# Performance work log

Measured on AMD Instinct MI355X. Metric: run time of the kernel, lower is better.

Reference implementation:

```python
import jax, jax.numpy as jnp
import numpy as np

INTER, COMMAND, MOTOR = 128, 64, 32
UNITS = MOTOR + COMMAND + INTER  # neuron order: motor, command, inter
SENSORY = 64
SENSORY_FANOUT, INTER_FANOUT = 16, 16
REC_CMD_SYN, MOTOR_FANIN = 128, 16
OUTPUT_LEN = 32
ODE_UNFOLDS = 6
EPS = 1e-8


def _build_wiring(rng):
    adj = np.zeros((UNITS, UNITS), np.float32)      # [pre, post]
    sadj = np.zeros((SENSORY, UNITS), np.float32)   # [sensory, post]
    motor = np.arange(0, MOTOR)
    command = np.arange(MOTOR, MOTOR + COMMAND)
    inter = np.arange(MOTOR + COMMAND, UNITS)
    pol = lambda: rng.choice(np.asarray([-1.0, 1.0], np.float32))
    for s in range(SENSORY):
        for d in rng.choice(inter, size=SENSORY_FANOUT, replace=False):
            sadj[s, d] = pol()
    for i in inter:
        for d in rng.choice(command, size=INTER_FANOUT, replace=False):
            adj[i, d] = pol()
    for _ in range(REC_CMD_SYN):
        adj[rng.choice(command), rng.choice(command)] = pol()
    for m in motor:
        for s in rng.choice(command, size=MOTOR_FANIN, replace=False):
            adj[s, m] = pol()
    return adj, sadj


def setup_inputs() -> dict:
    rng = np.random.default_rng(0)
    adj, sadj = _build_wiring(rng)
    u = lambda lo, hi, shp: jnp.asarray(rng.uniform(lo, hi, shp), jnp.float32)
    inp = {
        'inputs': jnp.asarray(rng.standard_normal((32, 32, SENSORY)), jnp.float32),
        'input_w': jnp.ones((SENSORY,), jnp.float32),
        'input_b': jnp.zeros((SENSORY,), jnp.float32),
        'sensory_mu': u(0.3, 0.8, (SENSORY, UNITS)),
        'sensory_sigma': u(3.0, 8.0, (SENSORY, UNITS)),
        'sensory_w': u(0.001, 1.0, (SENSORY, UNITS)),
        'sensory_erev': jnp.asarray(sadj),
        'sensory_mask': jnp.asarray(np.abs(sadj)),
        'mu': u(0.3, 0.8, (UNITS, UNITS)),
        'sigma': u(3.0, 8.0, (UNITS, UNITS)),
        'w': u(0.001, 1.0, (UNITS, UNITS)),
        'erev': jnp.asarray(adj),
        'mask': jnp.asarray(np.abs(adj)),
        'gleak': u(0.001, 1.0, (UNITS,)),
        'vleak': u(-0.2, 0.2, (UNITS,)),
        'cm': u(0.4, 0.6, (UNITS,)),
        'output_w': jnp.ones((MOTOR,), jnp.float32),
        'output_b': jnp.zeros((MOTOR,), jnp.float32),
        'dense_w': jnp.asarray(rng.standard_normal((MOTOR, OUTPUT_LEN)) / np.sqrt(MOTOR), jnp.float32),
        'dense_b': jnp.zeros((OUTPUT_LEN,), jnp.float32),
    }
    return inp


def reference(inputs, input_w, input_b, sensory_mu, sensory_sigma, sensory_w,
              sensory_erev, sensory_mask, mu, sigma, w, erev, mask,
              gleak, vleak, cm, output_w, output_b, dense_w, dense_b):
    # affine input mapping (per sensory feature)
    x = inputs * input_w + input_b  # [B,T,S]
    cm_t = cm * ODE_UNFOLDS        # cm / (elapsed_time / unfolds), elapsed_time=1

    def step(v, xt):  # v: [B,U], xt: [B,S]
        s_act = sensory_w * jax.nn.sigmoid(sensory_sigma * (xt[:, :, None] - sensory_mu)) * sensory_mask  # [B,S,U]
        w_num_s = jnp.sum(s_act * sensory_erev, axis=1)  # [B,U]
        w_den_s = jnp.sum(s_act, axis=1)
        for _ in range(ODE_UNFOLDS):
            w_act = w * jax.nn.sigmoid(sigma * (v[:, :, None] - mu)) * mask  # [B,U,U]
            num = cm_t * v + gleak * vleak + jnp.sum(w_act * erev, axis=1) + w_num_s
            den = cm_t + gleak + jnp.sum(w_act, axis=1) + w_den_s
            v = num / (den + EPS)
        return v, v

    v0 = jnp.zeros((x.shape[0], UNITS), x.dtype)
    _, vs = jax.lax.scan(step, v0, jnp.moveaxis(x, 1, 0))  # [T,B,U]
    motor = vs[..., :MOTOR] * output_w + output_b          # [T,B,M]
    out = jnp.einsum('tbm,mo->bto', motor, dense_w) + dense_b  # [B,T,OUT]
    return out
```

## Files before the change

### kernel.cpp

```cpp
#include <hip/hip_runtime.h>


#define U_N 224
#define S_N 64
#define T_N 32
#define M_N 32
#define C_N 64
#define I_N 128
#define O_N 32
#define NUF 6
#define TJT (T_N * NUF)
#define ELLS 24
#define ELLC 64
#define CCK 12
#define PFD 16
#define EPSV 1e-8f
#define L2E  1.44269504088896340736f

#define OFF_S2I   0
#define OFF_I2C   12288
#define OFF_CC    28672
#define OFF_M2T   31744
#define OFF_CNT   33792
#define OFF_CONST 34112
#define OFF_DYN   34816

#if __has_builtin(__builtin_amdgcn_rcpf)
#define RCPF(x) __builtin_amdgcn_rcpf(x)
#else
#define RCPF(x) (1.0f / (x))
#endif
#if __has_builtin(__builtin_amdgcn_exp2f)
#define EXP2F(x) __builtin_amdgcn_exp2f(x)
#else
#define EXP2F(x) exp2f(x)
#endif

__device__ __forceinline__ float bfu(unsigned short b) {
    return __uint_as_float(((unsigned int)b) << 16);
}
template <bool BF>
__device__ __forceinline__ float ld(const void* p, int i) {
    if (BF) return bfu(((const unsigned short*)p)[i]);
    return ((const float*)p)[i];
}
__device__ __forceinline__ unsigned short f2bf(float f) {
    unsigned int u = __float_as_uint(f);
    u += 0x7FFFu + ((u >> 16) & 1u);
    return (unsigned short)(u >> 16);
}
template <bool BF>
__device__ __forceinline__ void st_out(void* p, int i, float v) {
    if (BF) ((unsigned short*)p)[i] = f2bf(v);
    else    ((float*)p)[i] = v;
}
__device__ __forceinline__ float sigm2(float t) {
    return RCPF(1.0f + EXP2F(t));
}

template <bool BF>
__device__ void build_body(float* ws,
    const void* g_smu, const void* g_ssig, const void* g_sw,
    const void* g_serev, const void* g_smask,
    const void* g_mu, const void* g_sig, const void* g_w,
    const void* g_erev, const void* g_mask,
    const void* g_gleak, const void* g_vleak, const void* g_cm)
{
    const int tid = threadIdx.x;
    const int gt = blockIdx.x * 256 + tid;
    const int stride = gridDim.x * 256;
    int* cnt = (int*)(ws + OFF_CNT);
    if (gt < U_N) {
        float g = ld<BF>(g_gleak, gt);
        float cmt = ld<BF>(g_cm, gt) * (float)NUF;
        ws[OFF_CONST + gt] = cmt;
        ws[OFF_CONST + U_N + gt] = g * ld<BF>(g_vleak, gt);
        ws[OFF_CONST + 2 * U_N + gt] = cmt + g + EPSV;
    }
    float4* ws4 = (float4*)ws;
    for (int idx = gt; idx < U_N * U_N; idx += stride) {
        if (ld<BF>(g_mask, idx) != 0.f) {
            int pre = idx / U_N, post = idx - pre * U_N;
            float sg = ld<BF>(g_sig, idx) * L2E;
            float smu = sg * ld<BF>(g_mu, idx);
            float we = ld<BF>(g_w, idx) * ld<BF>(g_erev, idx);
            if (post < M_N) {
                int s = atomicAdd(&cnt[256 + post], 1);
                if (s < 16) ws4[OFF_M2T / 4 + s * M_N + post] =
                    make_float4(sg, smu, we, __int_as_float(pre - M_N));
            } else if (post < M_N + C_N) {
                int c = post - M_N;
                if (pre >= M_N + C_N) {
                    int s = atomicAdd(&cnt[128 + c], 1);
                    if (s < ELLC) ws4[OFF_I2C / 4 + c * ELLC + s] =
                        make_float4(sg, smu, we, __int_as_float(pre - M_N - C_N));
                } else {
                    int s = atomicAdd(&cnt[192 + c], 1);
                    if (s < CCK) ws4[OFF_CC / 4 + c * CCK + s] =
                        make_float4(sg, smu, we, __int_as_float(pre - M_N));
                }
            }
        }
    }
    for (int idx = gt; idx < S_N * U_N; idx += stride) {
        if (ld<BF>(g_smask, idx) != 0.f) {
            int pre = idx / U_N;
            int i = (idx - pre * U_N) - (M_N + C_N);
            if (i >= 0) {
                int s = atomicAdd(&cnt[i], 1);
                if (s < ELLS) {
                    float sg = ld<BF>(g_ssig, idx) * L2E;
                    ws4[OFF_S2I / 4 + i * ELLS + s] = make_float4(
                        sg, sg * ld<BF>(g_smu, idx),
                        ld<BF>(g_sw, idx) * ld<BF>(g_serev, idx),
                        __int_as_float(pre));
                }
            }
        }
    }
}

__global__ __launch_bounds__(256) void k_build(
    const void* sniff, const void* g_smu, const void* g_ssig, const void* g_sw,
    const void* g_serev, const void* g_smask, const void* g_mu,
    const void* g_sig, const void* g_w, const void* g_erev, const void* g_mask,
    const void* g_gleak, const void* g_vleak, const void* g_cm, float* ws)
{
    unsigned w0 = *(const unsigned int*)sniff;
    if (w0 == 0x3F800000u)
        build_body<false>(ws, g_smu, g_ssig, g_sw, g_serev, g_smask, g_mu,
                          g_sig, g_w, g_erev, g_mask, g_gleak, g_vleak, g_cm);
    else
        build_body<true>(ws, g_smu, g_ssig, g_sw, g_serev, g_smask, g_mu,
                         g_sig, g_w, g_erev, g_mask, g_gleak, g_vleak, g_cm);
}

template <bool BF>
__device__ void inter_body(float* ws, const void* g_inputs,
                           const void* g_in_w, const void* g_in_b)
{
    __shared__ float xs[T_N][S_N];
    const int tid = threadIdx.x, b = blockIdx.x;
    for (int g = tid; g < T_N * S_N; g += 256) {
        int t = g >> 6, s = g & 63;
        xs[t][s] = ld<BF>(g_inputs, (b * T_N + t) * S_N + s) *
                       ld<BF>(g_in_w, s) + ld<BF>(g_in_b, s);
    }
    const int iOwn = tid >> 1, lane2 = tid & 1;
    const float4* ws4 = (const float4*)ws;
    int n = ((const int*)(ws + OFF_CNT))[iOwn];
    float pSg[12], pMu[12], pW[12]; int pPre[12];
    #pragma unroll
    for (int k = 0; k < 12; ++k) {
        int s = lane2 + (k << 1);
        if (s < n) {
            float4 q = ws4[OFF_S2I / 4 + iOwn * ELLS + s];
            pSg[k] = q.x; pMu[k] = q.y; pW[k] = q.z; pPre[k] = __float_as_int(q.w);
        } else { pSg[k] = 0.f; pMu[k] = 0.f; pW[k] = 0.f; pPre[k] = 0; }
    }
    int kB = (n + 1) >> 1;
    #pragma unroll
    for (int off = 1; off < 64; off <<= 1) {
        int o = __shfl_xor(kB, off, 64); kB = (o > kB) ? o : kB;
    }
    kB = __builtin_amdgcn_readfirstlane(kB);
    const float cmtI = ws[OFF_CONST + M_N + C_N + iOwn];
    const float baseI = ws[OFF_CONST + U_N + M_N + C_N + iOwn];
    const float cgeI = ws[OFF_CONST + 2 * U_N + M_N + C_N + iOwn];
    __syncthreads();
    float* wVI = ws + OFF_DYN + (size_t)b * TJT * I_N;
    float vi = 0.f;
    for (int t = 0; t < T_N; ++t) {
        float accS = 0.f, accD = 0.f;
        #pragma unroll
        for (int k = 0; k < 12; ++k) {
            if (k < kB) {
                float xv = xs[t][pPre[k]];
                float sg = sigm2(fmaf(-pSg[k], xv, pMu[k]));
                float wv = pW[k] * sg;
                accS += wv; accD += fabsf(wv);
            }
        }
        accS += __shfl_xor(accS, 1, 2);
        accD += __shfl_xor(accD, 1, 2);
        float rden = RCPF(cgeI + accD);
        float A = cmtI * rden, Bv = (baseI + accS) * rden;
        #pragma unroll
        for (int j = 0; j < NUF; ++j) {
            if (lane2 == 0) wVI[(t * NUF + j) * I_N + iOwn] = vi;
            vi = fmaf(A, vi, Bv);
        }
    }
}

__global__ __launch_bounds__(256) void k_inter(
    const void* sniff, const void* g_inputs, const void* g_in_w,
    const void* g_in_b, float* ws)
{
    unsigned w0 = *(const unsigned int*)sniff;
    if (w0 == 0x3F800000u) inter_body<false>(ws, g_inputs, g_in_w, g_in_b);
    else                   inter_body<true>(ws, g_inputs, g_in_w, g_in_b);
}

__global__ __launch_bounds__(512) void k_i2c(float* ws)
{
    __shared__ float  vi_s[8 * I_N];
    __shared__ float2 scs[8 * C_N];
    const int tid = threadIdx.x, b = blockIdx.x, tj0 = blockIdx.y * 8;
    const int B = gridDim.x;
    const float* wVI = ws + OFF_DYN + ((size_t)b * TJT + tj0) * I_N;
    float2* wSC = (float2*)(ws + OFF_DYN + (size_t)B * TJT * I_N) +
                  ((size_t)b * (TJT + PFD) + tj0) * C_N;
    for (int g = tid; g < 8 * I_N; g += 512) vi_s[g] = wVI[g];
    const int cOwn = tid >> 3, lane8 = tid & 7;
    int n = ((const int*)(ws + OFF_CNT))[128 + cOwn];
    const float4* ws4 = (const float4*)ws;
    float pSg[8], pMu[8], pW[8]; int pPre[8];
    #pragma unroll
    for (int k = 0; k < 8; ++k) {
        int s = lane8 + (k << 3);
        if (s < n) {
            float4 q = ws4[OFF_I2C / 4 + cOwn * ELLC + s];
            pSg[k] = q.x; pMu[k] = q.y; pW[k] = q.z; pPre[k] = __float_as_int(q.w);
        } else { pSg[k] = 0.f; pMu[k] = 0.f; pW[k] = 0.f; pPre[k] = 0; }
    }
    int kB = (n + 7) >> 3;
    #pragma unroll
    for (int off = 1; off < 64; off <<= 1) {
        int o = __shfl_xor(kB, off, 64); kB = (o > kB) ? o : kB;
    }
    kB = __builtin_amdgcn_readfirstlane(kB);
    __syncthreads();
    for (int r = 0; r < 8; ++r) {
        const float* row = vi_s + r * I_N;
        float accS = 0.f, accD = 0.f;
        #pragma unroll
        for (int k = 0; k < 8; ++k) {
            if (k < kB) {
                float vv = row[pPre[k]];
                float sg = sigm2(fmaf(-pSg[k], vv, pMu[k]));
                float wv = pW[k] * sg;
                accS += wv; accD += fabsf(wv);
            }
        }
        accS += __shfl_xor(accS, 1, 8);
        accS += __shfl_xor(accS, 2, 8);
        accS += __shfl_xor(accS, 4, 8);
        accD += __shfl_xor(accD, 1, 8);
        accD += __shfl_xor(accD, 2, 8);
        accD += __shfl_xor(accD, 4, 8);
        if (lane8 == 0) scs[r * C_N + cOwn] = make_float2(accS, accD);
    }
    __syncthreads();
    wSC[tid] = scs[tid];
}

template <bool BF>
__device__ void cmdmo_body(float* ws, const void* g_ow, const void* g_ob,
                           const void* g_dw, const void* g_db,
                           void* __restrict__ g_out)
{
    __shared__ float  ct[TJT][C_N];
    __shared__ float2 mabc[24][M_N];
    __shared__ float  moutS[T_N][M_N];
    __shared__ float  dwS[M_N * O_N];
    const int tid = threadIdx.x, b = blockIdx.x, B = gridDim.x;
    for (int g = tid; g < M_N * O_N; g += 256) dwS[g] = ld<BF>(g_dw, g);

    if (tid < C_N) {
        const int lane = tid;
        int n = ((const int*)(ws + OFF_CNT))[192 + lane];
        const float4* ws4 = (const float4*)ws;
        float pSg[CCK], pMu[CCK], pW[CCK]; int pPre[CCK];
        #pragma unroll
        for (int k = 0; k < CCK; ++k) {
            if (k < n) {
                float4 q = ws4[OFF_CC / 4 + lane * CCK + k];
                pSg[k] = q.x; pMu[k] = q.y; pW[k] = q.z;
                pPre[k] = __float_as_int(q.w);
            } else { pSg[k] = 0.f; pMu[k] = 0.f; pW[k] = 0.f; pPre[k] = 0; }
        }
        int ccK = n;
        #pragma unroll
        for (int off = 1; off < 64; off <<= 1) {
            int o = __shfl_xor(ccK, off, 64); ccK = (o > ccK) ? o : ccK;
        }
        ccK = __builtin_amdgcn_readfirstlane(ccK);
        const float cmtC = ws[OFF_CONST + M_N + lane];
        const float baseC = ws[OFF_CONST + U_N + M_N + lane];
        const float cgeC = ws[OFF_CONST + 2 * U_N + M_N + lane];
        const float2* wSC = (const float2*)(ws + OFF_DYN + (size_t)B * TJT * I_N) +
                            (size_t)b * (TJT + PFD) * C_N + lane;
        float2 pf[PFD];
        #pragma unroll
        for (int k = 0; k < PFD; ++k) pf[k] = wSC[(size_t)k * C_N];
        float vC = 0.f;
        for (int tj0 = 0; tj0 < TJT; tj0 += PFD) {
            #pragma unroll
            for (int k = 0; k < PFD; ++k) {
                float2 sd = pf[k];
                pf[k] = wSC[(size_t)(tj0 + PFD + k) * C_N];
                ct[tj0 + k][lane] = vC;
                float accS = 0.f, accD = 0.f;
                #pragma unroll
                for (int kk = 0; kk < CCK; ++kk) {
                    if (kk < ccK) {
                        float vv = __shfl(vC, pPre[kk], 64);
                        float sg = sigm2(fmaf(-pSg[kk], vv, pMu[kk]));
                        float wv = pW[kk] * sg;
                        accS += wv; accD += fabsf(wv);
                    }
                }
                vC = fmaf(cmtC, vC, baseC + sd.x + accS) *
                     RCPF(cgeC + sd.y + accD);
            }
        }
    }
    __syncthreads();

    const int m = tid & 31, grp = tid >> 5;
    const float4* ws4 = (const float4*)ws;
    float4 q[16];
    #pragma unroll
    for (int k = 0; k < 16; ++k) q[k] = ws4[OFF_M2T / 4 + k * M_N + m];
    const float cmtM = ws[OFF_CONST + m];
    const float baseM = ws[OFF_CONST + U_N + m];
    const float cgeM = ws[OFF_CONST + 2 * U_N + m];
    float owR = 0.f, obR = 0.f, vM = 0.f;
    if (tid < M_N) { owR = ld<BF>(g_ow, tid); obR = ld<BF>(g_ob, tid); }
    for (int r = 0; r < 8; ++r) {
        #pragma unroll
        for (int z = 0; z < 3; ++z) {
            int tl = grp * 3 + z;
            const float* crow = ct[r * 24 + tl];
            float accS = 0.f, accD = 0.f;
            #pragma unroll
            for (int k = 0; k < 16; ++k) {
                float vv = crow[__float_as_int(q[k].w)];
                float sg = sigm2(fmaf(-q[k].x, vv, q[k].y));
                float wv = q[k].z * sg;
                accS += wv; accD += fabsf(wv);
            }
            float rden = RCPF(cgeM + accD);
            mabc[tl][m] = make_float2(cmtM * rden, (baseM + accS) * rden);
        }
        __syncthreads();
        if (tid < M_N) {
            #pragma unroll
            for (int tt = 0; tt < 4; ++tt) {
                #pragma unroll
                for (int j = 0; j < NUF; ++j) {
                    float2 ab = mabc[tt * NUF + j][tid];
                    vM = fmaf(ab.x, vM, ab.y);
                }
                moutS[r * 4 + tt][tid] = fmaf(vM, owR, obR);
            }
        }
        __syncthreads();
    }

    for (int g = tid; g < T_N * O_N; g += 256) {
        int t = g >> 5, o = g & 31;
        float acc = ld<BF>(g_db, o);
        #pragma unroll 8
        for (int mm = 0; mm < M_N; ++mm)
            acc += moutS[t][mm] * dwS[mm * O_N + o];
        st_out<BF>(g_out, (b * T_N + t) * O_N + o, acc);
    }
}

__global__ __launch_bounds__(256) void k_cmdmo(
    const void* sniff, float* ws, const void* g_ow, const void* g_ob,
    const void* g_dw, const void* g_db, void* __restrict__ g_out)
{
    unsigned w0 = *(const unsigned int*)sniff;
    if (w0 == 0x3F800000u) cmdmo_body<false>(ws, g_ow, g_ob, g_dw, g_db, g_out);
    else                   cmdmo_body<true>(ws, g_ow, g_ob, g_dw, g_db, g_out);
}

#define MONO_NT 640
#define CH  4
#define NCH (T_N / CH)
#define TJ  (CH * NUF)
#define KI  8
#define KS  6

struct SmemM {
    float cmt[U_N], base[U_N], cge[U_N];
    float4 m2t[16][M_N];
    float mout[T_N][M_N];
    union {
        struct {
            unsigned short ell_c[C_N][ELLC];
            unsigned short ell_s[I_N][ELLS];
            float4 cc[C_N][CCK];
            int cnt_c[C_N], cnt_s[I_N], cnt_cc[C_N], cnt_m[M_N];
        } b;
        struct {
            float  x[CH][S_N];
            float  Vi[TJ][I_N];
            float2 sc[2][TJ][C_N];
            float  ctraj[TJ][C_N];
            float2 mAB[TJ][M_N];
        } r;
    } u;
};

template <bool BF>
__device__ void mono_body(SmemM& sm,
    const void* g_inputs, const void* g_in_w, const void* g_in_b,
    const void* g_smu, const void* g_ssig, const void* g_sw,
    const void* g_serev, const void* g_smask,
    const void* g_mu, const void* g_sig, const void* g_w,
    const void* g_erev, const void* g_mask,
    const void* g_gleak, const void* g_vleak, const void* g_cm,
    const void* g_ow, const void* g_ob, const void* g_dw, const void* g_db,
    void* __restrict__ g_out)
{
    const int tid = threadIdx.x;
    const int b = blockIdx.x;
    const int p = tid - 64;
    const bool wp = (p >= 0 && p < 512);
    const bool isMo = (p >= 512 && p < 512 + M_N);

    if (tid < U_N) {
        float g = ld<BF>(g_gleak, tid);
        float cmt = ld<BF>(g_cm, tid) * (float)NUF;
        sm.cmt[tid] = cmt;
        sm.base[tid] = g * ld<BF>(g_vleak, tid);
        sm.cge[tid] = cmt + g + EPSV;
    }
    if (tid < C_N) { sm.u.b.cnt_c[tid] = 0; sm.u.b.cnt_cc[tid] = 0; }
    if (tid < I_N) sm.u.b.cnt_s[tid] = 0;
    if (tid < M_N) sm.u.b.cnt_m[tid] = 0;
    if (tid < 512) sm.m2t[tid >> 5][tid & 31] =
        make_float4(0.f, 0.f, 0.f, __int_as_float(0));
    __syncthreads();

    for (int idx = tid; idx < U_N * U_N; idx += MONO_NT) {
        if (ld<BF>(g_mask, idx) != 0.f) {
            int pre = idx / U_N;
            int post = idx - pre * U_N;
            if (post < M_N) {
                int s = atomicAdd(&sm.u.b.cnt_m[post], 1);
                if (s < 16) {
                    float sg = ld<BF>(g_sig, idx) * L2E;
                    float we = ld<BF>(g_w, idx) * ld<BF>(g_erev, idx);
                    sm.m2t[s][post] = make_float4(sg, sg * ld<BF>(g_mu, idx),
                                                  we, __int_as_float(pre - M_N));
                }
            } else if (post < M_N + C_N) {
                int c = post - M_N;
                if (pre >= M_N + C_N) {
                    int s = atomicAdd(&sm.u.b.cnt_c[c], 1);
                    if (s < ELLC) sm.u.b.ell_c[c][s] = (unsigned short)idx;
                } else {
                    int s = atomicAdd(&sm.u.b.cnt_cc[c], 1);
                    if (s < CCK) {
                        float sg = ld<BF>(g_sig, idx) * L2E;
                        float we = ld<BF>(g_w, idx) * ld<BF>(g_erev, idx);
                        sm.u.b.cc[c][s] = make_float4(sg, sg * ld<BF>(g_mu, idx),
                                                      we, __int_as_float(pre - M_N));
                    }
                }
            }
        }
    }
    for (int idx = tid; idx < S_N * U_N; idx += MONO_NT) {
        if (ld<BF>(g_smask, idx) != 0.f) {
            int pre = idx / U_N;
            int i = (idx - pre * U_N) - (M_N + C_N);
            if (i >= 0) {
                int s = atomicAdd(&sm.u.b.cnt_s[i], 1);
                if (s < ELLS) sm.u.b.ell_s[i][s] = (unsigned short)idx;
            }
        }
    }
    __syncthreads();

    const int cOwn = wp ? (p >> 3) : 0, lane8 = wp ? (p & 7) : 0;
    const int iOwn = wp ? (p >> 2) : 0, lane4 = wp ? (p & 3) : 0;
    float iSg[KI], iMu[KI], iW[KI]; int iPre[KI]; int kWi = 0;
    {
        int n = wp ? min(sm.u.b.cnt_c[cOwn], ELLC) : 0;
        #pragma unroll
        for (int k = 0; k < KI; ++k) {
            int s = lane8 + (k << 3);
            iSg[k] = 0.f; iMu[k] = 0.f; iW[k] = 0.f; iPre[k] = 0;
            if (s < n) {
                int flat = sm.u.b.ell_c[cOwn][s];
                float sg = ld<BF>(g_sig, flat) * L2E;
                iSg[k] = sg; iMu[k] = sg * ld<BF>(g_mu, flat);
                iW[k] = ld<BF>(g_w, flat) * ld<BF>(g_erev, flat);
                iPre[k] = flat / U_N - (M_N + C_N);
            }
        }
        kWi = (n + 7) >> 3;
    }
    float sSg[KS], sMu[KS], sW[KS]; int sPre[KS]; int kWs = 0;
    {
        int n = wp ? min(sm.u.b.cnt_s[iOwn], ELLS) : 0;
        #pragma unroll
        for (int k = 0; k < KS; ++k) {
            int s = lane4 + (k << 2);
            sSg[k] = 0.f; sMu[k] = 0.f; sW[k] = 0.f; sPre[k] = 0;
            if (s < n) {
                int flat = sm.u.b.ell_s[iOwn][s];
                float sg = ld<BF>(g_ssig, flat) * L2E;
                sSg[k] = sg; sMu[k] = sg * ld<BF>(g_smu, flat);
                sW[k] = ld<BF>(g_sw, flat) * ld<BF>(g_serev, flat);
                sPre[k] = flat / U_N;
            }
        }
        kWs = (n + 3) >> 2;
    }
    #pragma unroll
    for (int off = 1; off < 64; off <<= 1) {
        int o = __shfl_xor(kWi, off, 64); kWi = (o > kWi) ? o : kWi;
        int q2 = __shfl_xor(kWs, off, 64); kWs = (q2 > kWs) ? q2 : kWs;
    }
    kWi = __builtin_amdgcn_readfirstlane(kWi);
    kWs = __builtin_amdgcn_readfirstlane(kWs);

    float kSg[CCK], kMu[CCK], kW[CCK]; int kPre[CCK]; int ccK = 0;
    float cmtC = 0.f, baseC = 0.f, cgeC = 0.f;
    if (tid < C_N) {
        int n = min(sm.u.b.cnt_cc[tid], CCK);
        #pragma unroll
        for (int k = 0; k < CCK; ++k) {
            if (k < n) {
                float4 q3 = sm.u.b.cc[tid][k];
                kSg[k] = q3.x; kMu[k] = q3.y; kW[k] = q3.z;
                kPre[k] = __float_as_int(q3.w);
            } else { kSg[k] = 0.f; kMu[k] = 0.f; kW[k] = 0.f; kPre[k] = 0; }
        }
        ccK = n;
        #pragma unroll
        for (int off = 1; off < 64; off <<= 1) {
            int o = __shfl_xor(ccK, off, 64);
            ccK = (o > ccK) ? o : ccK;
        }
        ccK = __builtin_amdgcn_readfirstlane(ccK);
        cmtC = sm.cmt[M_N + tid]; baseC = sm.base[M_N + tid];
        cgeC = sm.cge[M_N + tid];
    }
    const float cmtI = sm.cmt[M_N + C_N + iOwn];
    const float baseI = sm.base[M_N + C_N + iOwn];
    const float cgeI = sm.cge[M_N + C_N + iOwn];
    float owR = 0.f, obR = 0.f;
    if (isMo) { owR = ld<BF>(g_ow, p - 512); obR = ld<BF>(g_ob, p - 512); }
    __syncthreads();

    if (wp && p < CH * S_N) {
        int tt = p >> 6, s = p & 63;
        sm.u.r.x[tt][s] = ld<BF>(g_inputs, (b * T_N + tt) * S_N + s) *
                              ld<BF>(g_in_w, s) + ld<BF>(g_in_b, s);
    }
    __syncthreads();

    float vInt = 0.f;
    float vCmd = 0.f;
    float vMot = 0.f;

    for (int i = 0; i <= NCH; ++i) {
        if (tid < C_N) {
            if (i >= 1) {
                const float2* scb = &sm.u.r.sc[(i - 1) & 1][0][0];
                for (int tj = 0; tj < TJ / 2; ++tj) {
                    sm.u.r.ctraj[tj][tid] = vCmd;
                    float accS = 0.f, accD = 0.f;
                    #pragma unroll
                    for (int k = 0; k < CCK; ++k) {
                        if (k < ccK) {
                            float vv = __shfl(vCmd, kPre[k], 64);
                            float sg = sigm2(fmaf(-kSg[k], vv, kMu[k]));
                            float wv = kW[k] * sg;
                            accS += wv; accD += fabsf(wv);
                        }
                    }
                    float2 sd = scb[tj * C_N + tid];
                    vCmd = fmaf(cmtC, vCmd, baseC + sd.x + accS) *
                           RCPF(cgeC + sd.y + accD);
                }
            }
        } else if (wp) {
            if (i < NCH) {
                float vi = vInt;
                for (int tt = 0; tt < CH; ++tt) {
                    float accS = 0.f, accD = 0.f;
                    #pragma unroll
                    for (int k = 0; k < KS; ++k) {
                        if (k < kWs) {
                            float xv = sm.u.r.x[tt][sPre[k]];
                            float sg = sigm2(fmaf(-sSg[k], xv, sMu[k]));
                            float wv = sW[k] * sg;
                            accS += wv; accD += fabsf(wv);
                        }
                    }
                    accS += __shfl_xor(accS, 1, 4); accS += __shfl_xor(accS, 2, 4);
                    accD += __shfl_xor(accD, 1, 4); accD += __shfl_xor(accD, 2, 4);
                    float rden = RCPF(cgeI + accD);
                    float A = cmtI * rden;
                    float Bv = (baseI + accS) * rden;
                    #pragma unroll
                    for (int j = 0; j < NUF; ++j) {
                        if (lane4 == 0) sm.u.r.Vi[tt * NUF + j][iOwn] = vi;
                        vi = fmaf(A, vi, Bv);
                    }
                }
                vInt = vi;
            }
        } else if (isMo && i >= 2) {
            int m = p - 512, c = i - 2;
            for (int tt = 0; tt < CH; ++tt) {
                #pragma unroll
                for (int j = 0; j < NUF; ++j) {
                    float2 ab = sm.u.r.mAB[tt * NUF + j][m];
                    vMot = fmaf(ab.x, vMot, ab.y);
                }
                sm.mout[c * CH + tt][m] = fmaf(vMot, owR, obR);
            }
        }
        __syncthreads();

        if (tid < C_N) {
            if (i >= 1) {
                const float2* scb = &sm.u.r.sc[(i - 1) & 1][0][0];
                for (int tj = TJ / 2; tj < TJ; ++tj) {
                    sm.u.r.ctraj[tj][tid] = vCmd;
                    float accS = 0.f, accD = 0.f;
                    #pragma unroll
                    for (int k = 0; k < CCK; ++k) {
                        if (k < ccK) {
                            float vv = __shfl(vCmd, kPre[k], 64);
                            float sg = sigm2(fmaf(-kSg[k], vv, kMu[k]));
                            float wv = kW[k] * sg;
                            accS += wv; accD += fabsf(wv);
                        }
                    }
                    float2 sd = scb[tj * C_N + tid];
                    vCmd = fmaf(cmtC, vCmd, baseC + sd.x + accS) *
                           RCPF(cgeC + sd.y + accD);
                }
            }
        } else if (wp) {
            if (i < NCH) {
                float2* scw = &sm.u.r.sc[i & 1][0][0];
                for (int tj = 0; tj < TJ; ++tj) {
                    const float* vrow = &sm.u.r.Vi[tj][0];
                    float accS = 0.f, accD = 0.f;
                    #pragma unroll
                    for (int k = 0; k < KI; ++k) {
                        if (k < kWi) {
                            float vv = vrow[iPre[k]];
                            float sg = sigm2(fmaf(-iSg[k], vv, iMu[k]));
                            float wv = iW[k] * sg;
                            accS += wv; accD += fabsf(wv);
                        }
                    }
                    accS += __shfl_xor(accS, 1, 8);
                    accS += __shfl_xor(accS, 2, 8);
                    accS += __shfl_xor(accS, 4, 8);
                    accD += __shfl_xor(accD, 1, 8);
                    accD += __shfl_xor(accD, 2, 8);
                    accD += __shfl_xor(accD, 4, 8);
                    if (lane8 == 0) scw[tj * C_N + cOwn] = make_float2(accS, accD);
                }
            }
            if (i + 1 < NCH && p < CH * S_N) {
                int tt = p >> 6, s = p & 63;
                sm.u.r.x[tt][s] =
                    ld<BF>(g_inputs, (b * T_N + (i + 1) * CH + tt) * S_N + s) *
                        ld<BF>(g_in_w, s) + ld<BF>(g_in_b, s);
            }
        }
        __syncthreads();

        if (i >= 1) {
            for (int g = tid; g < TJ * M_N; g += MONO_NT) {
                int tj = g >> 5, m = g & 31;
                const float* crow = &sm.u.r.ctraj[tj][0];
                float accS = 0.f, accD = 0.f;
                #pragma unroll
                for (int k = 0; k < 16; ++k) {
                    float4 q4 = sm.m2t[k][m];
                    float vv = crow[__float_as_int(q4.w)];
                    float sg = sigm2(fmaf(-q4.x, vv, q4.y));
                    float wv = q4.z * sg;
                    accS += wv; accD += fabsf(wv);
                }
                float rden = RCPF(sm.cge[m] + accD);
                sm.u.r.mAB[tj][m] = make_float2(sm.cmt[m] * rden,
                                                (sm.base[m] + accS) * rden);
            }
        }
        __syncthreads();
    }

    if (isMo) {
        int m = p - 512, c = NCH - 1;
        for (int tt = 0; tt < CH; ++tt) {
            #pragma unroll
            for (int j = 0; j < NUF; ++j) {
                float2 ab = sm.u.r.mAB[tt * NUF + j][m];
                vMot = fmaf(ab.x, vMot, ab.y);
            }
            sm.mout[c * CH + tt][m] = fmaf(vMot, owR, obR);
        }
    }
    __syncthreads();

    for (int g = tid; g < T_N * O_N; g += MONO_NT) {
        int t = g >> 5, o = g & 31;
        float acc = ld<BF>(g_db, o);
        #pragma unroll 8
        for (int m = 0; m < M_N; ++m)
            acc += sm.mout[t][m] * ld<BF>(g_dw, m * O_N + o);
        st_out<BF>(g_out, (b * T_N + t) * O_N + o, acc);
    }
}

__global__ __launch_bounds__(MONO_NT) void ncp_mono(
    const void* i0,  const void* i1,  const void* i2,  const void* i3,
    const void* i4,  const void* i5,  const void* i6,  const void* i7,
    const void* i8,  const void* i9,  const void* i10, const void* i11,
    const void* i12, const void* i13, const void* i14, const void* i15,
    const void* i16, const void* i17, const void* i18, const void* i19,
    void* __restrict__ g_out)
{
    __shared__ SmemM sm;
    unsigned w0 = *(const unsigned int*)i1;
    if (w0 == 0x3F800000u)
        mono_body<false>(sm, i0, i1, i2, i3, i4, i5, i6, i7, i8, i9, i10, i11,
                         i12, i13, i14, i15, i16, i17, i18, i19, g_out);
    else
        mono_body<true>(sm, i0, i1, i2, i3, i4, i5, i6, i7, i8, i9, i10, i11,
                        i12, i13, i14, i15, i16, i17, i18, i19, g_out);
}

extern "C" void kernel_launch(void* const* d_in, const int* in_sizes, int n_in,
                              void* d_out, int out_size, void* d_ws, size_t ws_size,
                              hipStream_t stream) {
    (void)n_in; (void)out_size;
    const int B = in_sizes[0] / (T_N * S_N);
    float* ws = (float*)d_ws;
    const size_t req = ((size_t)OFF_DYN + (size_t)B * TJT * I_N +
                        (size_t)B * (TJT + PFD) * C_N * 2) * sizeof(float);
    if (d_ws != nullptr && ws_size >= req) {
        hipMemsetAsync((char*)d_ws + (size_t)OFF_CNT * sizeof(float), 0,
                       288 * sizeof(int), stream);
        k_build<<<dim3(16), dim3(256), 0, stream>>>(
            d_in[1], d_in[3], d_in[4], d_in[5], d_in[6], d_in[7], d_in[8],
            d_in[9], d_in[10], d_in[11], d_in[12], d_in[13], d_in[14],
            d_in[15], ws);
        k_inter<<<dim3(B), dim3(256), 0, stream>>>(
            d_in[1], d_in[0], d_in[1], d_in[2], ws);
        k_i2c<<<dim3(B, TJT / 8), dim3(512), 0, stream>>>(ws);
        k_cmdmo<<<dim3(B), dim3(256), 0, stream>>>(
            d_in[1], ws, d_in[16], d_in[17], d_in[18], d_in[19], d_out);
    } else {
        ncp_mono<<<dim3(B), dim3(MONO_NT), 0, stream>>>(
            d_in[0],  d_in[1],  d_in[2],  d_in[3],  d_in[4],  d_in[5],
            d_in[6],  d_in[7],  d_in[8],  d_in[9],  d_in[10], d_in[11],
            d_in[12], d_in[13], d_in[14], d_in[15], d_in[16], d_in[17],
            d_in[18], d_in[19], d_out);
    }
}
```

Measured before the change: 222.8 us.

## Stage command inputs in double-buffered LDS and restructure motor phase

The sequential command-neuron recurrence no longer uses a register prefetch ring from global memory. The other waves copy 48-step segments of precomputed sensory/inter contributions into double-buffered shared memory while wave 0 iterates. Neighbour voltages are now read from the shared ct array instead of cross-lane shuffles. The motor phase is rewritten to compute all per-step A/B coefficients in one parallel pass and then run the motor recurrence once, which removes eight rounds of block barriers. The build grid size also doubles. The trade-offs are LDS reads on the critical serial path in place of shuffles, and a larger shared-memory footprint.

```diff
diff --git a/kernel.cpp b/kernel.cpp
--- a/kernel.cpp
+++ b/kernel.cpp
@@ -10,10 +10,10 @@
 #define O_N 32
 #define NUF 6
 #define TJT (T_N * NUF)
+#define SEG 48
 #define ELLS 24
 #define ELLC 64
 #define CCK 12
-#define PFD 16
 #define EPSV 1e-8f
 #define L2E  1.44269504088896340736f
 
@@ -136,10 +136,10 @@
 }
 
 template <bool BF>
-__device__ void inter_body(float* ws, const void* g_inputs,
-                           const void* g_in_w, const void* g_in_b)
-{
-    __shared__ float xs[T_N][S_N];
+__device__ void inter_body(float (&xs)[T_N][S_N], float* ws,
+                           const void* g_inputs, const void* g_in_w,
+                           const void* g_in_b)
+{
     const int tid = threadIdx.x, b = blockIdx.x;
     for (int g = tid; g < T_N * S_N; g += 256) {
         int t = g >> 6, s = g & 63;
@@ -197,9 +197,10 @@
     const void* sniff, const void* g_inputs, const void* g_in_w,
     const void* g_in_b, float* ws)
 {
+    __shared__ float xs[T_N][S_N];
     unsigned w0 = *(const unsigned int*)sniff;
-    if (w0 == 0x3F800000u) inter_body<false>(ws, g_inputs, g_in_w, g_in_b);
-    else                   inter_body<true>(ws, g_inputs, g_in_w, g_in_b);
+    if (w0 == 0x3F800000u) inter_body<false>(xs, ws, g_inputs, g_in_w, g_in_b);
+    else                   inter_body<true>(xs, ws, g_inputs, g_in_w, g_in_b);
 }
 
 __global__ __launch_bounds__(512) void k_i2c(float* ws)
@@ -210,7 +211,7 @@
     const int B = gridDim.x;
     const float* wVI = ws + OFF_DYN + ((size_t)b * TJT + tj0) * I_N;
     float2* wSC = (float2*)(ws + OFF_DYN + (size_t)B * TJT * I_N) +
-                  ((size_t)b * (TJT + PFD) + tj0) * C_N;
+                  ((size_t)b * TJT + tj0) * C_N;
     for (int g = tid; g < 8 * I_N; g += 512) vi_s[g] = wVI[g];
     const int cOwn = tid >> 3, lane8 = tid & 7;
     int n = ((const int*)(ws + OFF_CNT))[128 + cOwn];
@@ -255,57 +256,67 @@
     wSC[tid] = scs[tid];
 }
 
+struct SmemC {
+    float ct[TJT][C_N];
+    union {
+        float2 sb[2][SEG][C_N];
+        float2 mAB[TJT][M_N];
+    } u;
+    float moutS[T_N][M_N];
+    float dwS[M_N * O_N];
+};
+
 template <bool BF>
-__device__ void cmdmo_body(float* ws, const void* g_ow, const void* g_ob,
-                           const void* g_dw, const void* g_db,
-                           void* __restrict__ g_out)
-{
-    __shared__ float  ct[TJT][C_N];
-    __shared__ float2 mabc[24][M_N];
-    __shared__ float  moutS[T_N][M_N];
-    __shared__ float  dwS[M_N * O_N];
+__device__ void cmdmo_body(SmemC& s, float* ws, const void* g_ow,
+                           const void* g_ob, const void* g_dw,
+                           const void* g_db, void* __restrict__ g_out)
+{
     const int tid = threadIdx.x, b = blockIdx.x, B = gridDim.x;
-    for (int g = tid; g < M_N * O_N; g += 256) dwS[g] = ld<BF>(g_dw, g);
-
+    const float2* wSC = (const float2*)(ws + OFF_DYN + (size_t)B * TJT * I_N) +
+                        (size_t)b * TJT * C_N;
+    for (int g = tid; g < M_N * O_N; g += 256) s.dwS[g] = ld<BF>(g_dw, g);
+    for (int g = tid; g < SEG * C_N; g += 256)
+        (&s.u.sb[0][0][0])[g] = wSC[g];
+
+    float pSg[CCK], pMu[CCK], pW[CCK]; int pPre[CCK]; int ccK = 0;
+    float cmtC = 0.f, baseC = 0.f, cgeC = 0.f;
     if (tid < C_N) {
-        const int lane = tid;
-        int n = ((const int*)(ws + OFF_CNT))[192 + lane];
+        int n = ((const int*)(ws + OFF_CNT))[192 + tid];
         const float4* ws4 = (const float4*)ws;
-        float pSg[CCK], pMu[CCK], pW[CCK]; int pPre[CCK];
         #pragma unroll
         for (int k = 0; k < CCK; ++k) {
             if (k < n) {
-                float4 q = ws4[OFF_CC / 4 + lane * CCK + k];
+                float4 q = ws4[OFF_CC / 4 + tid * CCK + k];
                 pSg[k] = q.x; pMu[k] = q.y; pW[k] = q.z;
                 pPre[k] = __float_as_int(q.w);
             } else { pSg[k] = 0.f; pMu[k] = 0.f; pW[k] = 0.f; pPre[k] = 0; }
         }
-        int ccK = n;
+        ccK = n;
         #pragma unroll
         for (int off = 1; off < 64; off <<= 1) {
             int o = __shfl_xor(ccK, off, 64); ccK = (o > ccK) ? o : ccK;
         }
         ccK = __builtin_amdgcn_readfirstlane(ccK);
-        const float cmtC = ws[OFF_CONST + M_N + lane];
-        const float baseC = ws[OFF_CONST + U_N + M_N + lane];
-        const float cgeC = ws[OFF_CONST + 2 * U_N + M_N + lane];
-        const float2* wSC = (const float2*)(ws + OFF_DYN + (size_t)B * TJT * I_N) +
-                            (size_t)b * (TJT + PFD) * C_N + lane;
-        float2 pf[PFD];
-        #pragma unroll
-        for (int k = 0; k < PFD; ++k) pf[k] = wSC[(size_t)k * C_N];
-        float vC = 0.f;
-        for (int tj0 = 0; tj0 < TJT; tj0 += PFD) {
-            #pragma unroll
-            for (int k = 0; k < PFD; ++k) {
-                float2 sd = pf[k];
-                pf[k] = wSC[(size_t)(tj0 + PFD + k) * C_N];
-                ct[tj0 + k][lane] = vC;
+        cmtC = ws[OFF_CONST + M_N + tid];
+        baseC = ws[OFF_CONST + U_N + M_N + tid];
+        cgeC = ws[OFF_CONST + 2 * U_N + M_N + tid];
+    }
+    __syncthreads();
+
+    float vC = 0.f;
+    for (int seg = 0; seg < 4; ++seg) {
+        if (tid < C_N) {
+            const int lane = tid;
+            const float2* scb = &s.u.sb[seg & 1][0][0];
+            for (int r = 0; r < SEG; ++r) {
+                const int tj = seg * SEG + r;
+                s.ct[tj][lane] = vC;
+                float2 sd = scb[r * C_N + lane];
                 float accS = 0.f, accD = 0.f;
                 #pragma unroll
                 for (int kk = 0; kk < CCK; ++kk) {
                     if (kk < ccK) {
-                        float vv = __shfl(vC, pPre[kk], 64);
+                        float vv = s.ct[tj][pPre[kk]];
                         float sg = sigm2(fmaf(-pSg[kk], vv, pMu[kk]));
                         float wv = pW[kk] * sg;
                         accS += wv; accD += fabsf(wv);
@@ -314,11 +325,15 @@
                 vC = fmaf(cmtC, vC, baseC + sd.x + accS) *
                      RCPF(cgeC + sd.y + accD);
             }
-        }
-    }
-    __syncthreads();
-
-    const int m = tid & 31, grp = tid >> 5;
+        } else if (seg < 3) {
+            float2* dst = &s.u.sb[(seg + 1) & 1][0][0];
+            const float2* src = wSC + (size_t)(seg + 1) * SEG * C_N;
+            for (int g = tid - 64; g < SEG * C_N; g += 192) dst[g] = src[g];
+        }
+        __syncthreads();
+    }
+
+    const int m = tid & 31;
     const float4* ws4 = (const float4*)ws;
     float4 q[16];
     #pragma unroll
@@ -326,45 +341,42 @@
     const float cmtM = ws[OFF_CONST + m];
     const float baseM = ws[OFF_CONST + U_N + m];
     const float cgeM = ws[OFF_CONST + 2 * U_N + m];
-    float owR = 0.f, obR = 0.f, vM = 0.f;
-    if (tid < M_N) { owR = ld<BF>(g_ow, tid); obR = ld<BF>(g_ob, tid); }
-    for (int r = 0; r < 8; ++r) {
-        #pragma unroll
-        for (int z = 0; z < 3; ++z) {
-            int tl = grp * 3 + z;
-            const float* crow = ct[r * 24 + tl];
-            float accS = 0.f, accD = 0.f;
+    for (int g = tid; g < TJT * M_N; g += 256) {
+        int tj = g >> 5;
+        const float* crow = s.ct[tj];
+        float accS = 0.f, accD = 0.f;
+        #pragma unroll
+        for (int k = 0; k < 16; ++k) {
+            float vv = crow[__float_as_int(q[k].w)];
+            float sg = sigm2(fmaf(-q[k].x, vv, q[k].y));
+            float wv = q[k].z * sg;
+            accS += wv; accD += fabsf(wv);
+        }
+        float rden = RCPF(cgeM + accD);
+        s.u.mAB[tj][m] = make_float2(cmtM * rden, (baseM + accS) * rden);
+    }
+    __syncthreads();
+
+    if (tid < M_N) {
+        float ow = ld<BF>(g_ow, tid), ob = ld<BF>(g_ob, tid);
+        float vM = 0.f;
+        for (int t = 0; t < T_N; ++t) {
             #pragma unroll
-            for (int k = 0; k < 16; ++k) {
-                float vv = crow[__float_as_int(q[k].w)];
-                float sg = sigm2(fmaf(-q[k].x, vv, q[k].y));
-                float wv = q[k].z * sg;
-                accS += wv; accD += fabsf(wv);
-            }
-            float rden = RCPF(cgeM + accD);
-            mabc[tl][m] = make_float2(cmtM * rden, (baseM + accS) * rden);
-        }
-        __syncthreads();
-        if (tid < M_N) {
-            #pragma unroll
-            for (int tt = 0; tt < 4; ++tt) {
-                #pragma unroll
-                for (int j = 0; j < NUF; ++j) {
-                    float2 ab = mabc[tt * NUF + j][tid];
-                    vM = fmaf(ab.x, vM, ab.y);
-                }
-                moutS[r * 4 + tt][tid] = fmaf(vM, owR, obR);
-            }
-        }
-        __syncthreads();
-    }
+            for (int j = 0; j < NUF; ++j) {
+                float2 ab = s.u.mAB[t * NUF + j][tid];
+                vM = fmaf(ab.x, vM, ab.y);
+            }
+            s.moutS[t][tid] = fmaf(vM, ow, ob);
+        }
+    }
+    __syncthreads();
 
     for (int g = tid; g < T_N * O_N; g += 256) {
         int t = g >> 5, o = g & 31;
         float acc = ld<BF>(g_db, o);
         #pragma unroll 8
         for (int mm = 0; mm < M_N; ++mm)
-            acc += moutS[t][mm] * dwS[mm * O_N + o];
+            acc += s.moutS[t][mm] * s.dwS[mm * O_N + o];
         st_out<BF>(g_out, (b * T_N + t) * O_N + o, acc);
     }
 }
@@ -373,9 +385,10 @@
     const void* sniff, float* ws, const void* g_ow, const void* g_ob,
     const void* g_dw, const void* g_db, void* __restrict__ g_out)
 {
+    __shared__ SmemC s;
     unsigned w0 = *(const unsigned int*)sniff;
-    if (w0 == 0x3F800000u) cmdmo_body<false>(ws, g_ow, g_ob, g_dw, g_db, g_out);
-    else                   cmdmo_body<true>(ws, g_ow, g_ob, g_dw, g_db, g_out);
+    if (w0 == 0x3F800000u) cmdmo_body<false>(s, ws, g_ow, g_ob, g_dw, g_db, g_out);
+    else                   cmdmo_body<true>(s, ws, g_ow, g_ob, g_dw, g_db, g_out);
 }
 
 #define MONO_NT 640
@@ -745,11 +758,11 @@
     const int B = in_sizes[0] / (T_N * S_N);
     float* ws = (float*)d_ws;
     const size_t req = ((size_t)OFF_DYN + (size_t)B * TJT * I_N +
-                        (size_t)B * (TJT + PFD) * C_N * 2) * sizeof(float);
+                        (size_t)B * TJT * C_N * 2) * sizeof(float);
     if (d_ws != nullptr && ws_size >= req) {
         hipMemsetAsync((char*)d_ws + (size_t)OFF_CNT * sizeof(float), 0,
                        288 * sizeof(int), stream);
-        k_build<<<dim3(16), dim3(256), 0, stream>>>(
+        k_build<<<dim3(32), dim3(256), 0, stream>>>(
             d_in[1], d_in[3], d_in[4], d_in[5], d_in[6], d_in[7], d_in[8],
             d_in[9], d_in[10], d_in[11], d_in[12], d_in[13], d_in[14],
             d_in[15], ws);
```

Result: no change. 225.4 us (+1.2%).
